# Kernel tuning notes

Measured on AMD Instinct MI355X. Metric: run time of the kernel, lower is better.

## Reference

```python
import jax, jax.numpy as jnp
import numpy as np

B, DIM, FMAP = 32, 256, 32
HEADS, DK, DV = 8, 32, 64
N = FMAP * FMAP
SCALE = DK ** -0.5
EPS = 1e-5


def _bn(x, g, b):
    # training-mode BatchNorm2d: biased batch stats over (B, H, W)
    m = x.mean(axis=(0, 2, 3), keepdims=True)
    v = x.var(axis=(0, 2, 3), keepdims=True)
    return (x - m) * jax.lax.rsqrt(v + EPS) * g[None, :, None, None] + b[None, :, None, None]


def _conv1x1(x, W):
    # 1x1 conv, no bias: [O,C] x [B,C,H,W] -> [B,O,H,W]
    return jnp.einsum('oc,bchw->bohw', W, x)


def _make_pos_indices():
    r = np.arange(FMAP)
    pos = np.stack(np.meshgrid(r, r, indexing='ij'), axis=-1).reshape(-1, 2)  # [N,2]
    rel = np.abs(pos[:, None, :] - pos[None, :, :])  # [N,N,2]
    return (rel[..., 0] * FMAP + rel[..., 1]).astype(np.int32)


def setup_inputs() -> dict:
    key = jax.random.key(0)
    ks = jax.random.split(key, 16)
    s = 0.02
    return {
        'x': jax.random.normal(ks[0], (B, DIM, FMAP, FMAP), jnp.float32),
        'Wq': jax.random.normal(ks[1], (HEADS * DK, DIM), jnp.float32) * s,
        'gamma_q': jax.random.uniform(ks[2], (HEADS * DK,), jnp.float32, 0.5, 1.5),
        'beta_q': jax.random.normal(ks[3], (HEADS * DK,), jnp.float32) * 0.1,
        'Wk': jax.random.normal(ks[4], (HEADS * DK, DIM), jnp.float32) * s,
        'gamma_k': jax.random.uniform(ks[5], (HEADS * DK,), jnp.float32, 0.5, 1.5),
        'beta_k': jax.random.normal(ks[6], (HEADS * DK,), jnp.float32) * 0.1,
        'Wv': jax.random.normal(ks[7], (HEADS * DV, DIM), jnp.float32) * s,
        'gamma_v': jax.random.uniform(ks[8], (HEADS * DV,), jnp.float32, 0.5, 1.5),
        'beta_v': jax.random.normal(ks[9], (HEADS * DV,), jnp.float32) * 0.1,
        'Wo': jax.random.normal(ks[10], (DIM, HEADS * DV), jnp.float32) * s,
        'b_o': jax.random.normal(ks[11], (DIM,), jnp.float32) * 0.1,
        'gamma_o': jax.random.uniform(ks[12], (DIM,), jnp.float32, 0.5, 1.5),
        'beta_o': jax.random.normal(ks[13], (DIM,), jnp.float32) * 0.1,
        'pos_table': jax.random.normal(ks[14], (N, HEADS), jnp.float32) * 0.02,
        'pos_indices': jnp.asarray(_make_pos_indices()),
    }


def reference(x, Wq, gamma_q, beta_q, Wk, gamma_k, beta_k, Wv, gamma_v, beta_v,
              Wo, b_o, gamma_o, beta_o, pos_table, pos_indices):
    b = x.shape[0]
    q = _bn(_conv1x1(x, Wq), gamma_q, beta_q)
    k = _bn(_conv1x1(x, Wk), gamma_k, beta_k)
    v = _bn(_conv1x1(x, Wv), gamma_v, beta_v)

    def to_heads(t):
        bb, c, H, W = t.shape  # b (h d) H W -> b h (H W) d
        return t.reshape(bb, HEADS, c // HEADS, H * W).transpose(0, 1, 3, 2)

    q, k, v = to_heads(q), to_heads(k), to_heads(v)
    dots = jnp.einsum('bhid,bhjd->bhij', q, k) * SCALE  # [b,h,N,N]
    bias = pos_table[pos_indices]                        # gather -> [N,N,h]
    dots = dots + jnp.transpose(bias, (2, 0, 1))[None] / SCALE
    attn = jax.nn.softmax(dots, axis=-1)
    out = jnp.einsum('bhij,bhjd->bhid', attn, v)         # [b,h,N,dv]
    out = out.transpose(0, 1, 3, 2).reshape(b, HEADS * DV, FMAP, FMAP)
    out = jax.nn.gelu(out, approximate=False)
    out = _conv1x1(out, Wo) + b_o[None, :, None, None]
    return _bn(out, gamma_o, beta_o)
```

## Files before the change

### kernel.cpp

```cpp
#include <hip/hip_runtime.h>
#include <stdint.h>


typedef unsigned int uint;
typedef unsigned short ushort;

typedef __bf16 bf16x8 __attribute__((ext_vector_type(8)));
typedef short  shortx4 __attribute__((ext_vector_type(4)));
typedef float  floatx4 __attribute__((ext_vector_type(4)));

__device__ __forceinline__ float bf2f(ushort u){ uint t = ((uint)u)<<16; float f; __builtin_memcpy(&f,&t,4); return f; }
__device__ __forceinline__ ushort f2bf(float f){ uint u; __builtin_memcpy(&u,&f,4); return (ushort)((u + 0x7fffu + ((u>>16)&1u))>>16); }
__device__ __forceinline__ uint pack2(float a, float b){ return (uint)f2bf(a) | ((uint)f2bf(b)<<16); }
__device__ __forceinline__ uint fbits(float f){ uint u; __builtin_memcpy(&u,&f,4); return u; }
__device__ __forceinline__ float asf(uint u){ float f; __builtin_memcpy(&f,&u,4); return f; }
__device__ __forceinline__ uint4 cvt8(const float* p){
  float4 a = *(const float4*)p; float4 b = *(const float4*)(p+4);
  uint4 r; r.x = pack2(a.x,a.y); r.y = pack2(a.z,a.w); r.z = pack2(b.x,b.y); r.w = pack2(b.z,b.w);
  return r;
}

__device__ __forceinline__ floatx4 mfma32(bf16x8 a, bf16x8 b, floatx4 c){
  return __builtin_amdgcn_mfma_f32_16x16x32_bf16(a,b,c,0,0,0);
}
__device__ __forceinline__ floatx4 mfma16(shortx4 a, shortx4 b, floatx4 c){
  return __builtin_amdgcn_mfma_f32_16x16x16bf16_1k(a,b,c,0,0,0);
}

#define OFF_KB   16777216u
#define OFF_VT   33554432u
#define OFF_BIAS 67108864u
#define OFF_XT   83886080u
#define OFF_WBF  100663296u
#define OFF_SQK  101187584u
#define OFF_GT   83886080u
#define OFF_SUM  117440512u
#define OFF_OSUM 117448704u
#define OFF_AB   117450752u
#define WS_NEED  117460992u

__global__ __launch_bounds__(256) void k_prep(const float* __restrict__ x,
    const float* __restrict__ Wq, const float* __restrict__ Wk, const float* __restrict__ Wv,
    const float* __restrict__ pt,
    ushort* __restrict__ xT, ushort* __restrict__ wbf, ushort* __restrict__ bias){
  __shared__ ushort tr[64*66];
  int bid = blockIdx.x;
  int tid = threadIdx.x;
  if (bid < 256){
    int idx = (bid*256 + tid)*4;
    const float* src; int off;
    if (idx < 65536){ src = Wq; off = idx; }
    else if (idx < 131072){ src = Wk; off = idx - 65536; }
    else { src = Wv; off = idx - 131072; }
    float4 f = *(const float4*)(src + off);
    uint2 o; o.x = pack2(f.x,f.y); o.y = pack2(f.z,f.w);
    *(uint2*)(wbf + idx) = o;
  } else if (bid < 2304){
    int b2 = bid - 256;
    int cb = (b2 & 3)*64;
    int nb = ((b2>>2)&15)*64;
    int b  = b2>>6;
    int cl = tid>>2, n0 = (tid&3)*16;
    const float* src = x + (((size_t)b*256 + cb + cl)<<10) + nb + n0;
    ushort u16[16];
    #pragma unroll
    for(int q4=0;q4<4;q4++){
      float4 f = *(const float4*)(src + q4*4);
      u16[q4*4+0]=f2bf(f.x); u16[q4*4+1]=f2bf(f.y); u16[q4*4+2]=f2bf(f.z); u16[q4*4+3]=f2bf(f.w);
    }
    #pragma unroll
    for(int j=0;j<16;j++) tr[(n0+j)*66 + cl] = u16[j];
    __syncthreads();
    int nl = tid>>2, c0 = (tid&3)*16;
    uint o2[8];
    #pragma unroll
    for(int k=0;k<8;k++) o2[k] = *(const uint*)&tr[nl*66 + c0 + k*2];
    ushort* dst = xT + (((size_t)b*1024 + nb + nl)<<8) + cb + c0;
    *(uint4*)dst     = *(uint4*)&o2[0];
    *(uint4*)(dst+8) = *(uint4*)&o2[4];
  } else {
    int t = (bid-2304)*256 + tid;
    int lane = t & 63;
    int jsub = (t>>6)&63;
    int isub = (t>>12)&63;
    int h = t>>18;
    int i  = isub*16 + (lane&15);
    int jb = jsub*16 + ((lane>>4)<<2);
    int r1 = i>>5, c1 = i&31;
    const float BS = 1.44269504088896f*5.65685424949238f;
    ushort o[4];
    #pragma unroll
    for(int r=0;r<4;r++){
      int j = jb + r;
      int dr = r1 - (j>>5); dr = dr<0 ? -dr : dr;
      int dc = c1 - (j&31); dc = dc<0 ? -dc : dc;
      o[r] = f2bf(pt[(dr*32+dc)*8 + h] * BS);
    }
    uint2 ow; ow.x = (uint)o[0] | ((uint)o[1]<<16); ow.y = (uint)o[2] | ((uint)o[3]<<16);
    ((uint2*)bias)[t] = ow;
  }
}

__global__ __launch_bounds__(256) void k_qkv(const ushort* __restrict__ xT,
    const ushort* __restrict__ wbf,
    ushort* __restrict__ qb, ushort* __restrict__ kb, ushort* __restrict__ vt,
    float2* __restrict__ sqk){
  __shared__ ushort smem[18432];
  ushort* Ax = smem;
  ushort* Aw = smem + 9216;
  int bid = blockIdx.x;
  int nt = bid & 7; int ot = (bid>>3)&7; int b = bid>>6;
  int nb = nt*128, ob = ot*128;
  int mode = (ob < 256) ? 0 : (ob < 512 ? 1 : 2);
  int t = threadIdx.x, w = t>>6, l = t&63;
  int wr = w>>1, wc = w&1;
  int sr = t>>1, sc = (t&1)*32;
  const ushort* xrow = xT + (((size_t)b*1024 + nb + sr)<<8) + sc;
  const ushort* wrow = wbf + (size_t)(ob + sr)*256 + sc;
  floatx4 acc[4][4];
  #pragma unroll
  for(int m=0;m<4;m++)
    #pragma unroll
    for(int nf=0;nf<4;nf++) acc[m][nf] = (floatx4){0.f,0.f,0.f,0.f};

  for(int kc=0;kc<4;kc++){
    #pragma unroll
    for(int q4=0;q4<4;q4++){
      *(uint4*)&Ax[sr*72 + sc + q4*8] = *(const uint4*)(xrow + kc*64 + q4*8);
      *(uint4*)&Aw[sr*72 + sc + q4*8] = *(const uint4*)(wrow + kc*64 + q4*8);
    }
    __syncthreads();
    const ushort* Abuf = (mode==2)? Aw : Ax;
    const ushort* Bbuf = (mode==2)? Ax : Aw;
    int arb = (mode==2)? wc*64 : wr*64;
    int brb = (mode==2)? wr*64 : wc*64;
    #pragma unroll
    for(int kk=0;kk<2;kk++){
      bf16x8 af[4], bfr[4];
      #pragma unroll
      for(int m=0;m<4;m++)  af[m]  = *(const bf16x8*)&Abuf[(arb + m*16 + (l&15))*72 + kk*32 + (l>>4)*8];
      #pragma unroll
      for(int nf=0;nf<4;nf++) bfr[nf] = *(const bf16x8*)&Bbuf[(brb + nf*16 + (l&15))*72 + kk*32 + (l>>4)*8];
      #pragma unroll
      for(int m=0;m<4;m++)
        #pragma unroll
        for(int nf=0;nf<4;nf++)
          acc[m][nf] = mfma32(af[m], bfr[nf], acc[m][nf]);
    }
    __syncthreads();
  }

  int contrib = (nt*32 + b)*2 + wr;
  if (mode < 2){
    #pragma unroll
    for(int nf=0;nf<4;nf++){
      int o = ob + wc*64 + nf*16 + (l&15);
      float s1=0.f, s2=0.f;
      #pragma unroll
      for(int m=0;m<4;m++){
        #pragma unroll
        for(int r=0;r<4;r++){
          float val = acc[m][nf][r];
          s1 += val; s2 += val*val;
        }
      }
      s1 += __shfl_xor(s1,16,64); s1 += __shfl_xor(s1,32,64);
      s2 += __shfl_xor(s2,16,64); s2 += __shfl_xor(s2,32,64);
      if (l < 16){
        float2 p; p.x = s1; p.y = s2;
        sqk[(size_t)o*512 + contrib] = p;
      }
    }
  } else {
    #pragma unroll
    for(int m=0;m<4;m++){
      #pragma unroll
      for(int r=0;r<4;r++){
        int o  = ob + wc*64 + m*16 + (l>>4)*4 + r;
        float s1=0.f, s2=0.f;
        #pragma unroll
        for(int nf=0;nf<4;nf++){
          float val = acc[m][nf][r];
          s1 += val; s2 += val*val;
        }
        s1 += __shfl_xor(s1,1,64); s1 += __shfl_xor(s1,2,64); s1 += __shfl_xor(s1,4,64); s1 += __shfl_xor(s1,8,64);
        s2 += __shfl_xor(s2,1,64); s2 += __shfl_xor(s2,2,64); s2 += __shfl_xor(s2,4,64); s2 += __shfl_xor(s2,8,64);
        if ((l&15)==0){
          float2 p; p.x = s1; p.y = s2;
          sqk[(size_t)o*512 + contrib] = p;
        }
      }
    }
  }

  ushort* ep = smem + w*4608;
  if (mode < 2){
    #pragma unroll
    for(int m=0;m<4;m++)
      #pragma unroll
      for(int nf=0;nf<4;nf++){
        int lo = nf*16 + (l&15);
        #pragma unroll
        for(int r=0;r<4;r++){
          int ln = m*16 + (l>>4)*4 + r;
          ep[ln*72 + lo] = f2bf(acc[m][nf][r]);
        }
      }
    ushort* outb = (mode==0)? qb : kb;
    #pragma unroll
    for(int p=0;p<8;p++){
      int rr = p*8 + (l>>3);
      int ci = (l&7)*8;
      uint4 v = *(const uint4*)&ep[rr*72 + ci];
      int n = nb + wr*64 + rr;
      int o = ob + wc*64 + ci;
      int oc = o & 255;
      int h = oc>>5, d = oc&31;
      *(uint4*)(outb + (((size_t)(b*8+h)<<10) + n)*32 + d) = v;
    }
  } else {
    #pragma unroll
    for(int m=0;m<4;m++)
      #pragma unroll
      for(int nf=0;nf<4;nf++){
        int ln = nf*16 + (l&15);
        #pragma unroll
        for(int r=0;r<4;r++){
          int lo = m*16 + (l>>4)*4 + r;
          ep[lo*72 + ln] = f2bf(acc[m][nf][r]);
        }
      }
    #pragma unroll
    for(int p=0;p<8;p++){
      int rr = p*8 + (l>>3);
      int ci = (l&7)*8;
      uint4 v = *(const uint4*)&ep[rr*72 + ci];
      int o  = ob + wc*64 + rr;
      int ov = o - 512;
      int h = ov>>6, dv = ov&63;
      int n = nb + wr*64 + ci;
      *(uint4*)(vt + ((((size_t)b*8 + h)*64 + dv)<<10) + n) = v;
    }
  }
}

__global__ __launch_bounds__(256) void k_coef(const float2* __restrict__ sqk,
    const float* gq, const float* bq, const float* gk, const float* bk,
    const float* gvp, const float* bvp, float* __restrict__ ab){
  __shared__ float red[4][2];
  int ch = blockIdx.x;
  int t = threadIdx.x, w = t>>6, l = t&63;
  float2 v0 = sqk[(size_t)ch*512 + t];
  float2 v1 = sqk[(size_t)ch*512 + 256 + t];
  float s1 = v0.x + v1.x, s2 = v0.y + v1.y;
  s1 += __shfl_xor(s1,1,64); s2 += __shfl_xor(s2,1,64);
  s1 += __shfl_xor(s1,2,64); s2 += __shfl_xor(s2,2,64);
  s1 += __shfl_xor(s1,4,64); s2 += __shfl_xor(s2,4,64);
  s1 += __shfl_xor(s1,8,64); s2 += __shfl_xor(s2,8,64);
  s1 += __shfl_xor(s1,16,64); s2 += __shfl_xor(s2,16,64);
  s1 += __shfl_xor(s1,32,64); s2 += __shfl_xor(s2,32,64);
  if (l==0){ red[w][0]=s1; red[w][1]=s2; }
  __syncthreads();
  if (t==0){
    float S1 = red[0][0]+red[1][0]+red[2][0]+red[3][0];
    float S2 = red[0][1]+red[1][1]+red[2][1]+red[3][1];
    float mean = S1 * (1.0f/32768.0f);
    float var  = S2 * (1.0f/32768.0f) - mean*mean;
    float inv  = rsqrtf(var + 1e-5f);
    float g, be, ex;
    if (ch < 256){ g = gq[ch]; be = bq[ch]; ex = 1.44269504088896f*0.17677669529664f; }
    else if (ch < 512){ g = gk[ch-256]; be = bk[ch-256]; ex = 1.0f; }
    else { g = gvp[ch-512]; be = bvp[ch-512]; ex = 1.0f; }
    ab[ch*2]   = g*inv*ex;
    ab[ch*2+1] = (be - mean*g*inv)*ex;
  }
}

__device__ __forceinline__ bf16x8 qprep(uint4 raw, const float* __restrict__ abq,
                                        const float* __restrict__ abk){
  uint w4[4] = {raw.x, raw.y, raw.z, raw.w};
  ushort o[8];
  #pragma unroll
  for(int p=0;p<4;p++){
    float lo = asf(w4[p]<<16), hi = asf(w4[p] & 0xffff0000u);
    float q0 = abq[p*4+0]*lo + abq[p*4+1];
    float q1 = abq[p*4+2]*hi + abq[p*4+3];
    o[p*2]   = f2bf(q0 * abk[p*4+0]);
    o[p*2+1] = f2bf(q1 * abk[p*4+2]);
  }
  bf16x8 r; __builtin_memcpy(&r, o, 16);
  return r;
}

__global__ __launch_bounds__(256) void k_attn(const ushort* __restrict__ qb, const ushort* __restrict__ kb,
    const ushort* __restrict__ vt, const ushort* __restrict__ bias,
    const float* __restrict__ ab, ushort* __restrict__ GT){
  __shared__ ushort smem[9216];
  ushort* kt  = smem;
  ushort* vtl = smem + 2560;
  ushort* gbuf = smem;
  int bid = blockIdx.x;
  int h = bid & 7;
  int itile = (bid>>3)&7;
  int b = bid>>6;
  int t = threadIdx.x, w = t>>6, l = t&63;
  int isub0 = itile*8 + w*2;
  size_t bh = (size_t)b*8 + h;

  const float* abq = ab + (size_t)(h*32 + (l>>4)*8)*2;
  const float* abk = ab + (size_t)(256 + h*32 + (l>>4)*8)*2;
  uint4 qr0 = *(const uint4*)(qb + ((bh<<10) + isub0*16 + (l&15))*32 + (l>>4)*8);
  uint4 qr1 = *(const uint4*)(qb + ((bh<<10) + (isub0+1)*16 + (l&15))*32 + (l>>4)*8);
  bf16x8 qf0 = qprep(qr0, abq, abk);
  bf16x8 qf1 = qprep(qr1, abq, abk);

  const shortx4 vones = { (short)0x3F80, (short)0x3F80, (short)0x3F80, (short)0x3F80 };
  floatx4 lf0 = {0.f,0.f,0.f,0.f}, lf1 = {0.f,0.f,0.f,0.f};
  floatx4 O0[4] = {{0.f,0.f,0.f,0.f},{0.f,0.f,0.f,0.f},{0.f,0.f,0.f,0.f},{0.f,0.f,0.f,0.f}};
  floatx4 O1[4] = {{0.f,0.f,0.f,0.f},{0.f,0.f,0.f,0.f},{0.f,0.f,0.f,0.f},{0.f,0.f,0.f,0.f}};
  int sr = t>>2, scq = t&3;
  const uint2* bp0 = (const uint2*)bias + (((size_t)h*64 + isub0)*64)*64 + l;
  const uint2* bp1 = bp0 + 64*64;

  for(int jt=0;jt<16;jt++){
    int jbase = jt*64;
    *(uint4*)&kt[sr*40 + scq*8] = *(const uint4*)(kb + ((bh<<10) + jbase + sr)*32 + scq*8);
    const ushort* vsrc = vt + ((bh*64 + sr)<<10) + jbase + scq*16;
    *(uint4*)&vtl[sr*72 + scq*16]     = *(const uint4*)vsrc;
    *(uint4*)&vtl[sr*72 + scq*16 + 8] = *(const uint4*)(vsrc + 8);
    __syncthreads();

    #pragma unroll
    for(int js=0;js<4;js++){
      uint2 bw0 = bp0[js*64];
      uint2 bw1 = bp1[js*64];
      bf16x8 kf = *(const bf16x8*)&kt[(js*16 + (l&15))*40 + (l>>4)*8];
      floatx4 c0 = { asf(bw0.x<<16), asf(bw0.x & 0xffff0000u), asf(bw0.y<<16), asf(bw0.y & 0xffff0000u) };
      floatx4 c1 = { asf(bw1.x<<16), asf(bw1.x & 0xffff0000u), asf(bw1.y<<16), asf(bw1.y & 0xffff0000u) };
      floatx4 S0 = mfma32(kf, qf0, c0);
      floatx4 S1 = mfma32(kf, qf1, c1);
      float a0 = __builtin_amdgcn_exp2f(S0[0]);
      float a1 = __builtin_amdgcn_exp2f(S0[1]);
      float a2 = __builtin_amdgcn_exp2f(S0[2]);
      float a3 = __builtin_amdgcn_exp2f(S0[3]);
      float b0 = __builtin_amdgcn_exp2f(S1[0]);
      float b1 = __builtin_amdgcn_exp2f(S1[1]);
      float b2 = __builtin_amdgcn_exp2f(S1[2]);
      float b3 = __builtin_amdgcn_exp2f(S1[3]);
      uint2 pu0, pu1;
      pu0.x = __builtin_amdgcn_perm(fbits(a1), fbits(a0), 0x07060302u);
      pu0.y = __builtin_amdgcn_perm(fbits(a3), fbits(a2), 0x07060302u);
      pu1.x = __builtin_amdgcn_perm(fbits(b1), fbits(b0), 0x07060302u);
      pu1.y = __builtin_amdgcn_perm(fbits(b3), fbits(b2), 0x07060302u);
      shortx4 p0, p1;
      __builtin_memcpy(&p0, &pu0, 8);
      __builtin_memcpy(&p1, &pu1, 8);
      lf0 = mfma16(vones, p0, lf0);
      lf1 = mfma16(vones, p1, lf1);
      #pragma unroll
      for(int d=0;d<4;d++){
        shortx4 vf = *(const shortx4*)&vtl[(d*16 + (l&15))*72 + js*16 + (l>>4)*4];
        O0[d] = mfma16(vf, p0, O0[d]);
        O1[d] = mfma16(vf, p1, O1[d]);
      }
    }
    bp0 += 256; bp1 += 256;
    __syncthreads();
  }

  float invl0 = 1.0f/lf0[0];
  float invl1 = 1.0f/lf1[0];

  #pragma unroll
  for(int ii=0;ii<2;ii++){
    float invl = ii ? invl1 : invl0;
    #pragma unroll
    for(int d=0;d<4;d++){
      floatx4 Ov = ii ? O1[d] : O0[d];
      const float* abv = ab + (size_t)(512 + h*64 + d*16 + (l>>4)*4)*2;
      float4 e01 = *(const float4*)abv;
      float4 e23 = *(const float4*)(abv + 4);
      float av[4] = {e01.x, e01.z, e23.x, e23.z};
      float bv[4] = {e01.y, e01.w, e23.y, e23.w};
      ushort gu[4];
      #pragma unroll
      for(int r=0;r<4;r++){
        float o = av[r]*(Ov[r]*invl) + bv[r];
        float g = 0.5f*o*(1.0f + erff(o*0.70710678118655f));
        gu[r] = f2bf(g);
      }
      uint2 gw; gw.x = (uint)gu[0] | ((uint)gu[1]<<16); gw.y = (uint)gu[2] | ((uint)gu[3]<<16);
      *(uint2*)&gbuf[w*2304 + (ii*16 + (l&15))*72 + d*16 + (l>>4)*4] = gw;
    }
  }
  __syncthreads();
  int ibase = itile*128 + w*32;
  #pragma unroll
  for(int p8=0;p8<4;p8++){
    int rl = (l>>3) + p8*8;
    int ck = l&7;
    uint4 g4 = *(uint4*)&gbuf[w*2304 + rl*72 + ck*8];
    int n = ibase + rl;
    *(uint4*)(GT + ((size_t)(b*1024 + n))*512 + h*64 + ck*8) = g4;
  }
}

__global__ __launch_bounds__(256) void k_oconv(const ushort* __restrict__ GT, const float* __restrict__ Wo,
    const float* __restrict__ bo, ushort* __restrict__ opre, float2* __restrict__ soc){
  __shared__ ushort Aw[64*40];
  __shared__ ushort Ag[64*40];
  int bid = blockIdx.x;
  int nt = bid & 15; int ot = (bid>>4)&3; int b = bid>>6;
  int nb = nt*64, ob = ot*64;
  int t = threadIdx.x, w = t>>6, l = t&63;
  int sr = t>>2, sc = (t&3)*8;
  const float*  wsrc = Wo + (size_t)(ob + sr)*512 + sc;
  const ushort* gsrc = GT + ((size_t)b*1024 + nb + sr)*512 + sc;
  floatx4 acc[4] = {{0.f,0.f,0.f,0.f},{0.f,0.f,0.f,0.f},{0.f,0.f,0.f,0.f},{0.f,0.f,0.f,0.f}};
  for(int kc=0;kc<16;kc++){
    *(uint4*)&Aw[sr*40+sc] = cvt8(wsrc + kc*32);
    *(uint4*)&Ag[sr*40+sc] = *(const uint4*)(gsrc + kc*32);
    __syncthreads();
    bf16x8 af = *(const bf16x8*)&Aw[(w*16 + (l&15))*40 + (l>>4)*8];
    #pragma unroll
    for(int ns=0;ns<4;ns++){
      bf16x8 bfv = *(const bf16x8*)&Ag[(ns*16 + (l&15))*40 + (l>>4)*8];
      acc[ns] = mfma32(af, bfv, acc[ns]);
    }
    __syncthreads();
  }
  int contrib = nt*32 + b;
  #pragma unroll
  for(int r_=0;r_<4;r_++){
    int o = ob + w*16 + (l>>4)*4 + r_;
    float bias_o = bo[o];
    float s1=0.f, s2=0.f;
    #pragma unroll
    for(int ns=0;ns<4;ns++){
      int n = nb + ns*16 + (l&15);
      float val = acc[ns][r_] + bias_o;
      opre[(((size_t)(b*256+o))<<10) + n] = f2bf(val);
      s1 += val; s2 += val*val;
    }
    s1 += __shfl_xor(s1,1,64); s1 += __shfl_xor(s1,2,64); s1 += __shfl_xor(s1,4,64); s1 += __shfl_xor(s1,8,64);
    s2 += __shfl_xor(s2,1,64); s2 += __shfl_xor(s2,2,64); s2 += __shfl_xor(s2,4,64); s2 += __shfl_xor(s2,8,64);
    if ((l&15)==0){
      float2 p; p.x = s1; p.y = s2;
      soc[(size_t)o*512 + contrib] = p;
    }
  }
}

__global__ __launch_bounds__(256) void k_ocoef(const float2* __restrict__ soc,
    const float* __restrict__ go, const float* __restrict__ beo, float* __restrict__ oc){
  __shared__ float red[4][2];
  int ch = blockIdx.x;
  int t = threadIdx.x, w = t>>6, l = t&63;
  float2 v0 = soc[(size_t)ch*512 + t];
  float2 v1 = soc[(size_t)ch*512 + 256 + t];
  float s1 = v0.x + v1.x, s2 = v0.y + v1.y;
  s1 += __shfl_xor(s1,1,64); s2 += __shfl_xor(s2,1,64);
  s1 += __shfl_xor(s1,2,64); s2 += __shfl_xor(s2,2,64);
  s1 += __shfl_xor(s1,4,64); s2 += __shfl_xor(s2,4,64);
  s1 += __shfl_xor(s1,8,64); s2 += __shfl_xor(s2,8,64);
  s1 += __shfl_xor(s1,16,64); s2 += __shfl_xor(s2,16,64);
  s1 += __shfl_xor(s1,32,64); s2 += __shfl_xor(s2,32,64);
  if (l==0){ red[w][0]=s1; red[w][1]=s2; }
  __syncthreads();
  if (t==0){
    float S1 = red[0][0]+red[1][0]+red[2][0]+red[3][0];
    float S2 = red[0][1]+red[1][1]+red[2][1]+red[3][1];
    float mean = S1 * (1.0f/32768.0f);
    float var  = S2 * (1.0f/32768.0f) - mean*mean;
    float inv  = rsqrtf(var + 1e-5f);
    float a = go[ch]*inv;
    oc[ch*2]   = a;
    oc[ch*2+1] = beo[ch] - mean*a;
  }
}

__global__ __launch_bounds__(256) void k_bnout(const ushort* __restrict__ opre, const float* __restrict__ oc,
    float* __restrict__ out){
  size_t e = ((size_t)blockIdx.x*256 + threadIdx.x)*4;
  int o = (int)((e>>10)&255);
  float a = oc[o*2], bb = oc[o*2+1];
  uint2 raw = *(const uint2*)(opre + e);
  float4 ov;
  ov.x = a*asf(raw.x<<16)           + bb;
  ov.y = a*asf(raw.x & 0xffff0000u) + bb;
  ov.z = a*asf(raw.y<<16)           + bb;
  ov.w = a*asf(raw.y & 0xffff0000u) + bb;
  *(float4*)(out + e) = ov;
}

extern "C" void kernel_launch(void* const* d_in, const int* in_sizes, int n_in,
                              void* d_out, int out_size, void* d_ws, size_t ws_size,
                              hipStream_t stream){
  (void)in_sizes; (void)n_in; (void)out_size;
  const float* x   = (const float*)d_in[0];
  const float* Wq  = (const float*)d_in[1];
  const float* gq  = (const float*)d_in[2];
  const float* bq  = (const float*)d_in[3];
  const float* Wk  = (const float*)d_in[4];
  const float* gk  = (const float*)d_in[5];
  const float* bk  = (const float*)d_in[6];
  const float* Wv  = (const float*)d_in[7];
  const float* gvp = (const float*)d_in[8];
  const float* bvp = (const float*)d_in[9];
  const float* Wo  = (const float*)d_in[10];
  const float* bo  = (const float*)d_in[11];
  const float* go  = (const float*)d_in[12];
  const float* beo = (const float*)d_in[13];
  const float* pt  = (const float*)d_in[14];

  char* ws = (char*)d_ws;
  if (ws_size < (size_t)WS_NEED) return;
  ushort* qb   = (ushort*)(ws);
  ushort* kb   = (ushort*)(ws + OFF_KB);
  ushort* vt   = (ushort*)(ws + OFF_VT);
  ushort* bias = (ushort*)(ws + OFF_BIAS);
  ushort* xT   = (ushort*)(ws + OFF_XT);
  ushort* wbf  = (ushort*)(ws + OFF_WBF);
  ushort* GT   = (ushort*)(ws + OFF_GT);
  ushort* opre = (ushort*)(ws);
  float2* sqk  = (float2*)(ws + OFF_SQK);
  float2* soc  = (float2*)(ws + OFF_KB);
  float* oc    = (float*)(ws + OFF_OSUM);
  float* ab    = (float*)(ws + OFF_AB);

  k_prep<<<10496,256,0,stream>>>(x, Wq, Wk, Wv, pt, xT, wbf, bias);
  k_qkv<<<2048,256,0,stream>>>(xT, wbf, qb, kb, vt, sqk);
  k_coef<<<1024,256,0,stream>>>(sqk, gq, bq, gk, bk, gvp, bvp, ab);
  k_attn<<<2048,256,0,stream>>>(qb, kb, vt, bias, ab, GT);
  k_oconv<<<2048,256,0,stream>>>(GT, Wo, bo, opre, soc);
  k_ocoef<<<256,256,0,stream>>>(soc, go, beo, oc);
  k_bnout<<<8192,256,0,stream>>>(opre, oc, (float*)d_out);
}
```

Baseline: 307.2 us.

## Double K-chunk in output conv, stage epilogue through LDS, raise MFMA priority

The output 1x1 conv kernel now loads a 64-wide K chunk per iteration instead of 32, which halves the number of barrier pairs. Its bf16 output is first staged in shared memory so that each row is written to global with 16-byte vector stores instead of scattered 2-byte stores. The attention inner loop is wrapped in s_setprio so waves that are issuing MFMAs are scheduled ahead of waves that are loading. The cost is more LDS per block, which may lower occupancy of the conv kernel.

Result: no change. 307.3 us (+0.0%).

```diff
diff --git a/kernel.cpp b/kernel.cpp
--- a/kernel.cpp
+++ b/kernel.cpp
@@ -330,6 +330,7 @@
     *(uint4*)&vtl[sr*72 + scq*16 + 8] = *(const uint4*)(vsrc + 8);
     __syncthreads();
 
+    __builtin_amdgcn_s_setprio(1);
     #pragma unroll
     for(int js=0;js<4;js++){
       uint2 bw0 = bp0[js*64];
@@ -364,6 +365,7 @@
         O1[d] = mfma16(vf, p1, O1[d]);
       }
     }
+    __builtin_amdgcn_s_setprio(0);
     bp0 += 256; bp1 += 256;
     __syncthreads();
   }
@@ -407,39 +409,46 @@
 
 __global__ __launch_bounds__(256) void k_oconv(const ushort* __restrict__ GT, const float* __restrict__ Wo,
     const float* __restrict__ bo, ushort* __restrict__ opre, float2* __restrict__ soc){
-  __shared__ ushort Aw[64*40];
-  __shared__ ushort Ag[64*40];
+  __shared__ ushort smem[18432];
+  ushort* Aw = smem;
+  ushort* Ag = smem + 9216;
   int bid = blockIdx.x;
   int nt = bid & 15; int ot = (bid>>4)&3; int b = bid>>6;
   int nb = nt*64, ob = ot*64;
   int t = threadIdx.x, w = t>>6, l = t&63;
-  int sr = t>>2, sc = (t&3)*8;
+  int sr = t>>2, sc = (t&3)*16;
   const float*  wsrc = Wo + (size_t)(ob + sr)*512 + sc;
   const ushort* gsrc = GT + ((size_t)b*1024 + nb + sr)*512 + sc;
   floatx4 acc[4] = {{0.f,0.f,0.f,0.f},{0.f,0.f,0.f,0.f},{0.f,0.f,0.f,0.f},{0.f,0.f,0.f,0.f}};
-  for(int kc=0;kc<16;kc++){
-    *(uint4*)&Aw[sr*40+sc] = cvt8(wsrc + kc*32);
-    *(uint4*)&Ag[sr*40+sc] = *(const uint4*)(gsrc + kc*32);
-    __syncthreads();
-    bf16x8 af = *(const bf16x8*)&Aw[(w*16 + (l&15))*40 + (l>>4)*8];
-    #pragma unroll
-    for(int ns=0;ns<4;ns++){
-      bf16x8 bfv = *(const bf16x8*)&Ag[(ns*16 + (l&15))*40 + (l>>4)*8];
-      acc[ns] = mfma32(af, bfv, acc[ns]);
-    }
-    __syncthreads();
-  }
+  for(int kc=0;kc<8;kc++){
+    *(uint4*)&Aw[sr*72+sc]   = cvt8(wsrc + kc*64);
+    *(uint4*)&Aw[sr*72+sc+8] = cvt8(wsrc + kc*64 + 8);
+    *(uint4*)&Ag[sr*72+sc]   = *(const uint4*)(gsrc + kc*64);
+    *(uint4*)&Ag[sr*72+sc+8] = *(const uint4*)(gsrc + kc*64 + 8);
+    __syncthreads();
+    #pragma unroll
+    for(int kk=0;kk<2;kk++){
+      bf16x8 af = *(const bf16x8*)&Aw[(w*16 + (l&15))*72 + kk*32 + (l>>4)*8];
+      #pragma unroll
+      for(int ns=0;ns<4;ns++){
+        bf16x8 bfv = *(const bf16x8*)&Ag[(ns*16 + (l&15))*72 + kk*32 + (l>>4)*8];
+        acc[ns] = mfma32(af, bfv, acc[ns]);
+      }
+    }
+    __syncthreads();
+  }
+  ushort* ep = smem + w*1152;
   int contrib = nt*32 + b;
   #pragma unroll
   for(int r_=0;r_<4;r_++){
-    int o = ob + w*16 + (l>>4)*4 + r_;
+    int oloc = w*16 + (l>>4)*4 + r_;
+    int o = ob + oloc;
     float bias_o = bo[o];
     float s1=0.f, s2=0.f;
     #pragma unroll
     for(int ns=0;ns<4;ns++){
-      int n = nb + ns*16 + (l&15);
       float val = acc[ns][r_] + bias_o;
-      opre[(((size_t)(b*256+o))<<10) + n] = f2bf(val);
+      ep[((l>>4)*4 + r_)*72 + ns*16 + (l&15)] = f2bf(val);
       s1 += val; s2 += val*val;
     }
     s1 += __shfl_xor(s1,1,64); s1 += __shfl_xor(s1,2,64); s1 += __shfl_xor(s1,4,64); s1 += __shfl_xor(s1,8,64);
@@ -448,6 +457,15 @@
       float2 p; p.x = s1; p.y = s2;
       soc[(size_t)o*512 + contrib] = p;
     }
+  }
+  {
+    int rr = l>>2, cseg = (l&3)*16;
+    uint4 v0 = *(const uint4*)&ep[rr*72 + cseg];
+    uint4 v1 = *(const uint4*)&ep[rr*72 + cseg + 8];
+    int o = ob + w*16 + rr;
+    ushort* dst = opre + (((size_t)(b*256+o))<<10) + nb + cseg;
+    *(uint4*)dst     = v0;
+    *(uint4*)(dst+8) = v1;
   }
 }
 
```
